# Performance work log

Hardware: AMD Instinct MI355X
Metric: run time of the kernel (lower is better)

## Reference

```python
import jax, jax.numpy as jnp
import numpy as np

N_NODES = 50000
N_EDGES = 800000
STATE_DIM = 128
H1 = 96
H2 = 64


def setup_inputs() -> dict:
    key = jax.random.key(0)
    ks = jax.random.split(key, 10)
    x = jax.random.normal(ks[0], (N_NODES, STATE_DIM), dtype=jnp.float32)
    edge_index = jax.random.randint(ks[1], (2, N_EDGES), 0, N_NODES, dtype=jnp.int64)
    # GCNConv weight [in, out] and bias
    W1 = jax.random.normal(ks[2], (STATE_DIM, H1), dtype=jnp.float32) / np.sqrt(STATE_DIM)
    b1 = jnp.zeros((H1,), dtype=jnp.float32)
    lw1 = jax.random.normal(ks[3], (H1, H1), dtype=jnp.float32) / np.sqrt(H1)
    lb1 = jax.random.normal(ks[4], (H1,), dtype=jnp.float32) * 0.01
    lw2 = jax.random.normal(ks[5], (H1, H2), dtype=jnp.float32) / np.sqrt(H1)
    lb2 = jax.random.normal(ks[6], (H2,), dtype=jnp.float32) * 0.01
    lw3 = jax.random.normal(ks[7], (H2, 1), dtype=jnp.float32) / np.sqrt(H2)
    lb3 = jax.random.normal(ks[8], (1,), dtype=jnp.float32) * 0.01
    return {"x": x, "edge_index": edge_index, "W1": W1, "b1": b1,
            "lw1": lw1, "lb1": lb1, "lw2": lw2, "lb2": lb2, "lw3": lw3, "lb3": lb3}


def reference(x, edge_index, W1, b1, lw1, lb1, lw2, lb2, lw3, lb3):
    N = x.shape[0]
    loop = jnp.arange(N, dtype=edge_index.dtype)
    src = jnp.concatenate([edge_index[0], loop])
    dst = jnp.concatenate([edge_index[1], loop])
    deg = jax.ops.segment_sum(jnp.ones_like(dst, dtype=x.dtype), dst, num_segments=N)
    dinv = jnp.where(deg > 0, jax.lax.rsqrt(jnp.maximum(deg, 1.0)), 0.0)
    norm = dinv[src] * dinv[dst]  # [E+N]
    h = x @ W1  # [N, H1] transform before propagation
    agg = jax.ops.segment_sum(h[src] * norm[:, None], dst, num_segments=N) + b1
    out = jax.nn.relu(agg)            # [N, H1]
    g = jnp.sum(out, axis=0)          # sum pooling over nodes -> [H1]
    g = jax.nn.relu(g @ lw1 + lb1)
    g = jax.nn.relu(g @ lw2 + lb2)
    return g @ lw3 + lb3              # [1]
```

## Files before the change

### kernel.cpp

```cpp
#include <hip/hip_runtime.h>
#include <stdint.h>

#define N_NODES 50000
#define N_EDGES 800000
#define D_IN 128
#define H1 96
#define H2 64
#define GEMM_NODES 32
#define GEMM_BLOCKS ((N_NODES + GEMM_NODES - 1) / GEMM_NODES)
#define COUNT_BLOCKS 2048
#define SCAN_BLK 256
#define N_SBLK ((N_NODES + SCAN_BLK - 1) / SCAN_BLK)
#define SCAT_BLOCKS 2048
#define SCALE_BLOCKS 512
#define AGG_BLOCKS 2048

__device__ __forceinline__ int xcd_range(int d) {
    return (int)(((unsigned long long)(unsigned)d * 687195ull) >> 32);
}

__global__ __launch_bounds__(256) void k1_gemm_count(const float* __restrict__ x,
                                                     const float* __restrict__ W1,
                                                     float* __restrict__ h,
                                                     const int* __restrict__ dst,
                                                     int* __restrict__ deg) {
    __shared__ float sx[GEMM_NODES * D_IN];
    int tid = threadIdx.x;

    if (blockIdx.x < GEMM_BLOCKS) {
        int base = blockIdx.x * GEMM_NODES;
        const float4* x4 = (const float4*)x;
        for (int i = tid; i < GEMM_NODES * D_IN / 4; i += 256) {
            int n = base + i / (D_IN / 4);
            if (n < N_NODES) ((float4*)sx)[i] = x4[(size_t)base * (D_IN / 4) + i];
        }
        __syncthreads();

        int fg = tid & 31;
        int ng = tid >> 5;

        float acc[4][3];
#pragma unroll
        for (int i = 0; i < 4; ++i)
#pragma unroll
            for (int j = 0; j < 3; ++j) acc[i][j] = 0.0f;

#pragma unroll 4
        for (int k = 0; k < D_IN; ++k) {
            float w0 = W1[k * H1 + fg];
            float w1 = W1[k * H1 + fg + 32];
            float w2 = W1[k * H1 + fg + 64];
#pragma unroll
            for (int i = 0; i < 4; ++i) {
                float xv = sx[(ng * 4 + i) * D_IN + k];
                acc[i][0] = fmaf(xv, w0, acc[i][0]);
                acc[i][1] = fmaf(xv, w1, acc[i][1]);
                acc[i][2] = fmaf(xv, w2, acc[i][2]);
            }
        }

#pragma unroll
        for (int i = 0; i < 4; ++i) {
            int n = base + ng * 4 + i;
            if (n < N_NODES) {
                h[(size_t)n * H1 + fg]      = acc[i][0];
                h[(size_t)n * H1 + fg + 32] = acc[i][1];
                h[(size_t)n * H1 + fg + 64] = acc[i][2];
            }
        }
    } else {
        int r = blockIdx.x & 7;
        int bid = blockIdx.x - GEMM_BLOCKS;
        int gid = (bid >> 3) * 256 + tid;
        int stride = (COUNT_BLOCKS >> 3) * 256;
        const int4* d4 = (const int4*)dst;
        for (int i = gid; i < N_EDGES / 4; i += stride) {
            int4 d = d4[i];
            if (xcd_range(d.x) == r) atomicAdd(&deg[d.x], 1);
            if (xcd_range(d.y) == r) atomicAdd(&deg[d.y], 1);
            if (xcd_range(d.z) == r) atomicAdd(&deg[d.z], 1);
            if (xcd_range(d.w) == r) atomicAdd(&deg[d.w], 1);
        }
    }
}

__global__ __launch_bounds__(SCAN_BLK) void deg_part_kernel(const int* __restrict__ deg,
                                                            int* __restrict__ block_sums) {
    __shared__ int s[SCAN_BLK];
    int t = threadIdx.x;
    int i = blockIdx.x * SCAN_BLK + t;
    s[t] = (i < N_NODES) ? deg[i] : 0;
    __syncthreads();
    for (int off = SCAN_BLK / 2; off > 0; off >>= 1) {
        if (t < off) s[t] += s[t + off];
        __syncthreads();
    }
    if (t == 0) block_sums[blockIdx.x] = s[0];
}

__global__ __launch_bounds__(SCAN_BLK) void block_scan_kernel(int* __restrict__ block_sums) {
    __shared__ int s[SCAN_BLK];
    int t = threadIdx.x;
    int v = (t < N_SBLK) ? block_sums[t] : 0;
    s[t] = v;
    __syncthreads();
    for (int off = 1; off < SCAN_BLK; off <<= 1) {
        int u = (t >= off) ? s[t - off] : 0;
        __syncthreads();
        s[t] += u;
        __syncthreads();
    }
    if (t < N_SBLK) block_sums[t] = s[t] - v;
}

__global__ __launch_bounds__(SCAN_BLK) void deg_scan_kernel(const int* __restrict__ deg,
                                                            const int* __restrict__ block_off,
                                                            int* __restrict__ row_start,
                                                            int* __restrict__ cursor,
                                                            float* __restrict__ dinv) {
    __shared__ int s[SCAN_BLK];
    int t = threadIdx.x;
    int i = blockIdx.x * SCAN_BLK + t;
    int v = (i < N_NODES) ? deg[i] : 0;
    s[t] = v;
    __syncthreads();
    for (int off = 1; off < SCAN_BLK; off <<= 1) {
        int u = (t >= off) ? s[t - off] : 0;
        __syncthreads();
        s[t] += u;
        __syncthreads();
    }
    int excl = s[t] - v + block_off[blockIdx.x];
    if (i < N_NODES) {
        row_start[i] = excl;
        cursor[i] = excl;
        dinv[i] = rsqrtf((float)v + 1.0f);
    }
    if (i == 0) row_start[N_NODES] = N_EDGES;
}

__global__ __launch_bounds__(256) void k2_scatter_scale(const int* __restrict__ src,
                                                        const int* __restrict__ dst,
                                                        int* __restrict__ cursor,
                                                        int* __restrict__ sorted_src,
                                                        float* __restrict__ h,
                                                        const float* __restrict__ dinv) {
    int tid = threadIdx.x;
    if (blockIdx.x < SCAT_BLOCKS) {
        int r = blockIdx.x & 7;
        int gid = (blockIdx.x >> 3) * 256 + tid;
        int stride = (SCAT_BLOCKS >> 3) * 256;
        const int4* s4p = (const int4*)src;
        const int4* d4p = (const int4*)dst;
        for (int i = gid; i < N_EDGES / 4; i += stride) {
            int4 sv = s4p[i];
            int4 dv = d4p[i];
            if (xcd_range(dv.x) == r) { int p = atomicAdd(&cursor[dv.x], 1); sorted_src[p] = sv.x; }
            if (xcd_range(dv.y) == r) { int p = atomicAdd(&cursor[dv.y], 1); sorted_src[p] = sv.y; }
            if (xcd_range(dv.z) == r) { int p = atomicAdd(&cursor[dv.z], 1); sorted_src[p] = sv.z; }
            if (xcd_range(dv.w) == r) { int p = atomicAdd(&cursor[dv.w], 1); sorted_src[p] = sv.w; }
        }
    } else {
        int bid = blockIdx.x - SCAT_BLOCKS;
        int gid = bid * 256 + tid;
        int stride = SCALE_BLOCKS * 256;
        float4* h4 = (float4*)h;
        const int TOT = N_NODES * (H1 / 4);
        for (int i = gid; i < TOT; i += stride) {
            int n = i / (H1 / 4);
            float dv = dinv[n];
            float4 v = h4[i];
            v.x *= dv; v.y *= dv; v.z *= dv; v.w *= dv;
            h4[i] = v;
        }
    }
}

__global__ __launch_bounds__(256) void agg_pool_kernel(const float* __restrict__ hs,
                                                       const int* __restrict__ row_start,
                                                       const int* __restrict__ sorted_src,
                                                       const float* __restrict__ dinv,
                                                       const float* __restrict__ b1,
                                                       float* __restrict__ g) {
    int tid = threadIdx.x;
    int grp = tid >> 7;
    int f = tid & 127;
    bool act = f < H1;
    float bf = act ? b1[f] : 0.0f;
    float gacc = 0.0f;

    for (int n = blockIdx.x * 2 + grp; n < N_NODES; n += gridDim.x * 2) {
        float acc = act ? hs[(size_t)n * H1 + f] : 0.0f;
        int e = row_start[n];
        int eend = row_start[n + 1];
        for (; e + 4 <= eend; e += 4) {
            int s0 = sorted_src[e];
            int s1 = sorted_src[e + 1];
            int s2 = sorted_src[e + 2];
            int s3 = sorted_src[e + 3];
            if (act) {
                float v0 = hs[(size_t)s0 * H1 + f];
                float v1 = hs[(size_t)s1 * H1 + f];
                float v2 = hs[(size_t)s2 * H1 + f];
                float v3 = hs[(size_t)s3 * H1 + f];
                acc += (v0 + v1) + (v2 + v3);
            }
        }
        for (; e < eend; ++e) {
            int s = sorted_src[e];
            if (act) acc += hs[(size_t)s * H1 + f];
        }
        if (act) gacc += fmaxf(fmaf(dinv[n], acc, bf), 0.0f);
    }

    __shared__ float sg[H1];
    if (grp == 0 && act) sg[f] = gacc;
    __syncthreads();
    if (grp == 1 && act) atomicAdd(&sg[f], gacc);
    __syncthreads();
    if (grp == 0 && act) atomicAdd(&g[f], sg[f]);
}

__global__ __launch_bounds__(256) void mlp_kernel(const float* __restrict__ g,
                           const float* __restrict__ lw1, const float* __restrict__ lb1,
                           const float* __restrict__ lw2, const float* __restrict__ lb2,
                           const float* __restrict__ lw3, const float* __restrict__ lb3,
                           float* __restrict__ out) {
    __shared__ float slw1[H1 * H1];
    __shared__ float slw2[H1 * H2];
    __shared__ float slw3[H2];
    __shared__ float sg[H1], v1[H1], v2[H2];
    int t = threadIdx.x;
    for (int i = t; i < H1 * H1 / 4; i += 256)
        ((float4*)slw1)[i] = ((const float4*)lw1)[i];
    for (int i = t; i < H1 * H2 / 4; i += 256)
        ((float4*)slw2)[i] = ((const float4*)lw2)[i];
    if (t < H2) slw3[t] = lw3[t];
    if (t < H1) sg[t] = g[t];
    __syncthreads();
    if (t < H1) {
        float a = lb1[t];
#pragma unroll 8
        for (int k = 0; k < H1; ++k) a = fmaf(sg[k], slw1[k * H1 + t], a);
        v1[t] = fmaxf(a, 0.0f);
    }
    __syncthreads();
    if (t < H2) {
        float a = lb2[t];
#pragma unroll 8
        for (int k = 0; k < H1; ++k) a = fmaf(v1[k], slw2[k * H2 + t], a);
        v2[t] = fmaxf(a, 0.0f);
    }
    __syncthreads();
    if (t == 0) {
        float a = lb3[0];
#pragma unroll 8
        for (int k = 0; k < H2; ++k) a = fmaf(v2[k], slw3[k], a);
        out[0] = a;
    }
}

extern "C" void kernel_launch(void* const* d_in, const int* in_sizes, int n_in,
                              void* d_out, int out_size, void* d_ws, size_t ws_size,
                              hipStream_t stream) {
    const float* x   = (const float*)d_in[0];
    const int*   ei  = (const int*)d_in[1];
    const float* W1  = (const float*)d_in[2];
    const float* b1  = (const float*)d_in[3];
    const float* lw1 = (const float*)d_in[4];
    const float* lb1 = (const float*)d_in[5];
    const float* lw2 = (const float*)d_in[6];
    const float* lb2 = (const float*)d_in[7];
    const float* lw3 = (const float*)d_in[8];
    const float* lb3 = (const float*)d_in[9];
    float* out = (float*)d_out;

    const int* src = ei;
    const int* dst = ei + N_EDGES;

    char* ws = (char*)d_ws;
    size_t off = 0;
    auto alloc = [&](size_t bytes) {
        char* p = ws + off;
        off = (off + bytes + 255) & ~(size_t)255;
        return p;
    };
    int*   deg        = (int*)alloc((size_t)N_NODES * sizeof(int));
    float* g          = (float*)alloc((size_t)H1 * sizeof(float));
    float* dinv       = (float*)alloc((size_t)N_NODES * sizeof(float));
    int*   row_start  = (int*)alloc((size_t)(N_NODES + 1) * sizeof(int));
    int*   cursor     = (int*)alloc((size_t)N_NODES * sizeof(int));
    int*   block_sums = (int*)alloc((size_t)N_SBLK * sizeof(int));
    int*   sorted_src = (int*)alloc((size_t)N_EDGES * sizeof(int));
    float* h          = (float*)alloc((size_t)N_NODES * H1 * sizeof(float));
    (void)ws_size;

    hipMemsetAsync(deg, 0, (char*)(g + H1) - (char*)deg, stream);

    k1_gemm_count<<<GEMM_BLOCKS + COUNT_BLOCKS, 256, 0, stream>>>(x, W1, h, dst, deg);

    deg_part_kernel<<<N_SBLK, SCAN_BLK, 0, stream>>>(deg, block_sums);
    block_scan_kernel<<<1, SCAN_BLK, 0, stream>>>(block_sums);
    deg_scan_kernel<<<N_SBLK, SCAN_BLK, 0, stream>>>(deg, block_sums, row_start, cursor, dinv);

    k2_scatter_scale<<<SCAT_BLOCKS + SCALE_BLOCKS, 256, 0, stream>>>(src, dst, cursor, sorted_src,
                                                                     h, dinv);

    agg_pool_kernel<<<AGG_BLOCKS, 256, 0, stream>>>(h, row_start, sorted_src, dinv, b1, g);

    mlp_kernel<<<1, 256, 0, stream>>>(g, lw1, lb1, lw2, lb2, lw3, lb3, out);
}
```

Baseline: 207.9 us.

## Pre-partition edges into per-XCD packed buckets during degree count

```diff
diff --git a/kernel.cpp b/kernel.cpp
--- a/kernel.cpp
+++ b/kernel.cpp
@@ -6,24 +6,28 @@
 #define D_IN 128
 #define H1 96
 #define H2 64
-#define GEMM_NODES 32
+#define GEMM_NODES 64
 #define GEMM_BLOCKS ((N_NODES + GEMM_NODES - 1) / GEMM_NODES)
-#define COUNT_BLOCKS 2048
+#define PART_BLOCKS 800
 #define SCAN_BLK 256
 #define N_SBLK ((N_NODES + SCAN_BLK - 1) / SCAN_BLK)
 #define SCAT_BLOCKS 2048
 #define SCALE_BLOCKS 512
 #define AGG_BLOCKS 2048
+#define CAP 112000
 
 __device__ __forceinline__ int xcd_range(int d) {
     return (int)(((unsigned long long)(unsigned)d * 687195ull) >> 32);
 }
 
-__global__ __launch_bounds__(256) void k1_gemm_count(const float* __restrict__ x,
-                                                     const float* __restrict__ W1,
-                                                     float* __restrict__ h,
-                                                     const int* __restrict__ dst,
-                                                     int* __restrict__ deg) {
+__global__ __launch_bounds__(256) void k1_gemm_partition(const float* __restrict__ x,
+                                                         const float* __restrict__ W1,
+                                                         float* __restrict__ h,
+                                                         const int* __restrict__ src,
+                                                         const int* __restrict__ dst,
+                                                         int* __restrict__ deg,
+                                                         int* __restrict__ pairs,
+                                                         int* __restrict__ bcnt) {
     __shared__ float sx[GEMM_NODES * D_IN];
     int tid = threadIdx.x;
 
@@ -39,9 +43,9 @@
         int fg = tid & 31;
         int ng = tid >> 5;
 
-        float acc[4][3];
+        float acc[8][3];
 #pragma unroll
-        for (int i = 0; i < 4; ++i)
+        for (int i = 0; i < 8; ++i)
 #pragma unroll
             for (int j = 0; j < 3; ++j) acc[i][j] = 0.0f;
 
@@ -51,8 +55,8 @@
             float w1 = W1[k * H1 + fg + 32];
             float w2 = W1[k * H1 + fg + 64];
 #pragma unroll
-            for (int i = 0; i < 4; ++i) {
-                float xv = sx[(ng * 4 + i) * D_IN + k];
+            for (int i = 0; i < 8; ++i) {
+                float xv = sx[(ng * 8 + i) * D_IN + k];
                 acc[i][0] = fmaf(xv, w0, acc[i][0]);
                 acc[i][1] = fmaf(xv, w1, acc[i][1]);
                 acc[i][2] = fmaf(xv, w2, acc[i][2]);
@@ -60,8 +64,8 @@
         }
 
 #pragma unroll
-        for (int i = 0; i < 4; ++i) {
-            int n = base + ng * 4 + i;
+        for (int i = 0; i < 8; ++i) {
+            int n = base + ng * 8 + i;
             if (n < N_NODES) {
                 h[(size_t)n * H1 + fg]      = acc[i][0];
                 h[(size_t)n * H1 + fg + 32] = acc[i][1];
@@ -69,17 +73,43 @@
             }
         }
     } else {
-        int r = blockIdx.x & 7;
+        __shared__ int lh[8];
+        __shared__ int lbase[8];
         int bid = blockIdx.x - GEMM_BLOCKS;
-        int gid = (bid >> 3) * 256 + tid;
-        int stride = (COUNT_BLOCKS >> 3) * 256;
-        const int4* d4 = (const int4*)dst;
-        for (int i = gid; i < N_EDGES / 4; i += stride) {
-            int4 d = d4[i];
-            if (xcd_range(d.x) == r) atomicAdd(&deg[d.x], 1);
-            if (xcd_range(d.y) == r) atomicAdd(&deg[d.y], 1);
-            if (xcd_range(d.z) == r) atomicAdd(&deg[d.z], 1);
-            if (xcd_range(d.w) == r) atomicAdd(&deg[d.w], 1);
+        const int4* s4p = (const int4*)src;
+        const int4* d4p = (const int4*)dst;
+        const int NQ = N_EDGES / 4;
+
+        for (int base = bid * 256; base < NQ; base += PART_BLOCKS * 256) {
+            int i = base + tid;
+            bool valid = i < NQ;
+            if (tid < 8) lh[tid] = 0;
+            __syncthreads();
+
+            int4 dv, sv;
+            int r0 = 0, r1 = 0, r2 = 0, r3 = 0, l0 = 0, l1 = 0, l2 = 0, l3 = 0;
+            if (valid) {
+                dv = d4p[i];
+                sv = s4p[i];
+                r0 = xcd_range(dv.x); l0 = atomicAdd(&lh[r0], 1);
+                r1 = xcd_range(dv.y); l1 = atomicAdd(&lh[r1], 1);
+                r2 = xcd_range(dv.z); l2 = atomicAdd(&lh[r2], 1);
+                r3 = xcd_range(dv.w); l3 = atomicAdd(&lh[r3], 1);
+                atomicAdd(&deg[dv.x], 1);
+                atomicAdd(&deg[dv.y], 1);
+                atomicAdd(&deg[dv.z], 1);
+                atomicAdd(&deg[dv.w], 1);
+            }
+            __syncthreads();
+            if (tid < 8) lbase[tid] = atomicAdd(&bcnt[tid], lh[tid]);
+            __syncthreads();
+            if (valid) {
+                pairs[r0 * CAP + lbase[r0] + l0] = ((dv.x - r0 * 6250) << 17) | sv.x;
+                pairs[r1 * CAP + lbase[r1] + l1] = ((dv.y - r1 * 6250) << 17) | sv.y;
+                pairs[r2 * CAP + lbase[r2] + l2] = ((dv.z - r2 * 6250) << 17) | sv.z;
+                pairs[r3 * CAP + lbase[r3] + l3] = ((dv.w - r3 * 6250) << 17) | sv.w;
+            }
+            __syncthreads();
         }
     }
 }
@@ -139,8 +169,8 @@
     if (i == 0) row_start[N_NODES] = N_EDGES;
 }
 
-__global__ __launch_bounds__(256) void k2_scatter_scale(const int* __restrict__ src,
-                                                        const int* __restrict__ dst,
+__global__ __launch_bounds__(256) void k3_scatter_scale(const int* __restrict__ pairs,
+                                                        const int* __restrict__ bcnt,
                                                         int* __restrict__ cursor,
                                                         int* __restrict__ sorted_src,
                                                         float* __restrict__ h,
@@ -148,17 +178,17 @@
     int tid = threadIdx.x;
     if (blockIdx.x < SCAT_BLOCKS) {
         int r = blockIdx.x & 7;
+        int cnt = bcnt[r];
+        const int* pb = pairs + r * CAP;
         int gid = (blockIdx.x >> 3) * 256 + tid;
         int stride = (SCAT_BLOCKS >> 3) * 256;
-        const int4* s4p = (const int4*)src;
-        const int4* d4p = (const int4*)dst;
-        for (int i = gid; i < N_EDGES / 4; i += stride) {
-            int4 sv = s4p[i];
-            int4 dv = d4p[i];
-            if (xcd_range(dv.x) == r) { int p = atomicAdd(&cursor[dv.x], 1); sorted_src[p] = sv.x; }
-            if (xcd_range(dv.y) == r) { int p = atomicAdd(&cursor[dv.y], 1); sorted_src[p] = sv.y; }
-            if (xcd_range(dv.z) == r) { int p = atomicAdd(&cursor[dv.z], 1); sorted_src[p] = sv.z; }
-            if (xcd_range(dv.w) == r) { int p = atomicAdd(&cursor[dv.w], 1); sorted_src[p] = sv.w; }
+        int rbase = r * 6250;
+        for (int i = gid; i < cnt; i += stride) {
+            int v = pb[i];
+            int d = rbase + (v >> 17);
+            int s = v & 0x1FFFF;
+            int p = atomicAdd(&cursor[d], 1);
+            sorted_src[p] = s;
         }
     } else {
         int bid = blockIdx.x - SCAT_BLOCKS;
@@ -287,24 +317,27 @@
     };
     int*   deg        = (int*)alloc((size_t)N_NODES * sizeof(int));
     float* g          = (float*)alloc((size_t)H1 * sizeof(float));
+    int*   bcnt       = (int*)alloc(8 * sizeof(int));
     float* dinv       = (float*)alloc((size_t)N_NODES * sizeof(float));
     int*   row_start  = (int*)alloc((size_t)(N_NODES + 1) * sizeof(int));
     int*   cursor     = (int*)alloc((size_t)N_NODES * sizeof(int));
     int*   block_sums = (int*)alloc((size_t)N_SBLK * sizeof(int));
     int*   sorted_src = (int*)alloc((size_t)N_EDGES * sizeof(int));
+    int*   pairs      = (int*)alloc((size_t)8 * CAP * sizeof(int));
     float* h          = (float*)alloc((size_t)N_NODES * H1 * sizeof(float));
     (void)ws_size;
 
-    hipMemsetAsync(deg, 0, (char*)(g + H1) - (char*)deg, stream);
-
-    k1_gemm_count<<<GEMM_BLOCKS + COUNT_BLOCKS, 256, 0, stream>>>(x, W1, h, dst, deg);
+    hipMemsetAsync(deg, 0, (char*)(bcnt + 8) - (char*)deg, stream);
+
+    k1_gemm_partition<<<GEMM_BLOCKS + PART_BLOCKS, 256, 0, stream>>>(x, W1, h, src, dst,
+                                                                     deg, pairs, bcnt);
 
     deg_part_kernel<<<N_SBLK, SCAN_BLK, 0, stream>>>(deg, block_sums);
     block_scan_kernel<<<1, SCAN_BLK, 0, stream>>>(block_sums);
     deg_scan_kernel<<<N_SBLK, SCAN_BLK, 0, stream>>>(deg, block_sums, row_start, cursor, dinv);
 
-    k2_scatter_scale<<<SCAT_BLOCKS + SCALE_BLOCKS, 256, 0, stream>>>(src, dst, cursor, sorted_src,
-                                                                     h, dinv);
+    k3_scatter_scale<<<SCAT_BLOCKS + SCALE_BLOCKS, 256, 0, stream>>>(pairs, bcnt, cursor,
+                                                                     sorted_src, h, dinv);
 
     agg_pool_kernel<<<AGG_BLOCKS, 256, 0, stream>>>(h, row_start, sorted_src, dinv, b1, g);
 
```

After: 216.8 us. 4.3% more time.
